# Kernel tuning notes

Measured on AMD Instinct MI355X. Metric: run time of the kernel, lower is better.

## Reference

```python
import jax, jax.numpy as jnp
import numpy as np

D_MODEL = 1024
NUM_HEADS = 16
D_K = D_MODEL // NUM_HEADS
THETA = 10000.0


def _rope(x, pos):
    # x: [B, H, T, d_k], pos: [T]
    inv_freq = 1.0 / (THETA ** (jnp.arange(0, D_K, 2, dtype=jnp.float32) / D_K))  # [d_k/2]
    ang = pos.astype(jnp.float32)[:, None] * inv_freq[None, :]                    # [T, d_k/2]
    cos = jnp.repeat(jnp.cos(ang), 2, axis=-1)                                    # [T, d_k]
    sin = jnp.repeat(jnp.sin(ang), 2, axis=-1)
    x = x.astype(jnp.float32)
    x0 = x[..., ::2]
    x1 = x[..., 1::2]
    rot = jnp.stack((-x1, x0), axis=-1).reshape(x.shape)  # rotate_half, interleaved
    return x * cos + rot * sin


def setup_inputs() -> dict:
    key = jax.random.key(0)
    k1, k2, k3 = jax.random.split(key, 3)
    B, T = 2, 2048
    sigma_qkv = float(np.sqrt(2.0 / (D_MODEL + 3 * D_MODEL)))
    sigma_out = float(np.sqrt(2.0 / (D_MODEL + D_MODEL)))
    return {
        "x": jax.random.normal(k1, (B, T, D_MODEL), dtype=jnp.float32),
        "w_qkv": jax.random.normal(k2, (3 * D_MODEL, D_MODEL), dtype=jnp.float32) * sigma_qkv,
        "w_out": jax.random.normal(k3, (D_MODEL, D_MODEL), dtype=jnp.float32) * sigma_out,
    }


def reference(x, w_qkv, w_out):
    B, T, _ = x.shape
    qkv = jnp.einsum("btd,ed->bte", x, w_qkv)                 # [B, T, 3*D]
    q, k, v = jnp.split(qkv, 3, axis=-1)

    def split_head(t):
        return t.reshape(B, T, NUM_HEADS, D_K).transpose(0, 2, 1, 3)  # [B, H, T, d_k]

    q, k, v = split_head(q), split_head(k), split_head(v)
    pos = jnp.arange(T)
    q = _rope(q, pos)
    k = _rope(k, pos)

    scores = jnp.einsum("bhqd,bhkd->bhqk", q, k) / jnp.sqrt(jnp.float32(D_K))
    causal = jnp.tril(jnp.ones((T, T), dtype=bool))            # True = keep
    scores = jnp.where(causal[None, None], scores, -jnp.inf)
    attn = jax.nn.softmax(scores, axis=-1)
    out = jnp.einsum("bhqk,bhkd->bhqd", attn, v)               # [B, H, T, d_k]
    out = out.transpose(0, 2, 1, 3).reshape(B, T, D_MODEL)
    return jnp.einsum("btd,ed->bte", out, w_out)
```

## Files before the change

### kernel.cpp

```cpp
#include <hip/hip_runtime.h>
#include <cstdint>
#include <cstddef>

#define BB 2
#define TT 2048
#define DMODEL 1024
#define NHEADS 16
#define DK 64

typedef short short8 __attribute__((ext_vector_type(8)));
typedef unsigned short ushort8 __attribute__((ext_vector_type(8)));
typedef float floatx4 __attribute__((ext_vector_type(4)));
typedef _Float16 half4 __attribute__((ext_vector_type(4)));
typedef float float2v __attribute__((ext_vector_type(2)));

#define MFMA_PV(A, B, C) __builtin_amdgcn_mfma_f32_16x16x16f16(A, B, C, 0, 0, 0)

__device__ __forceinline__ unsigned short f2bf(float f) {
    uint32_t u = __builtin_bit_cast(uint32_t, f);
    uint32_t r = (u + 0x7FFFu + ((u >> 16) & 1u)) >> 16;
    return (unsigned short)r;
}
__device__ __forceinline__ float bf2f(unsigned short s) {
    uint32_t u = ((uint32_t)s) << 16;
    return __builtin_bit_cast(float, u);
}

#define GLDS16(g, l) __builtin_amdgcn_global_load_lds( \
    (const __attribute__((address_space(1))) void*)(g), \
    (__attribute__((address_space(3))) void*)(l), 16, 0, 0)

__global__ void castk3(const float* __restrict__ x, unsigned short* __restrict__ xb,
                       const float* __restrict__ wq, unsigned short* __restrict__ wqb,
                       const float* __restrict__ wo, unsigned short* __restrict__ wob) {
    int bid = blockIdx.x;
    const float* in;
    unsigned short* out;
    int base;
    if (bid < 4096)       { in = x;  out = xb;  base = bid * 1024; }
    else if (bid < 7168)  { in = wq; out = wqb; base = (bid - 4096) * 1024; }
    else                  { in = wo; out = wob; base = (bid - 7168) * 1024; }
    int i = base + threadIdx.x * 4;
    float4 v = *(const float4*)(in + i);
    ushort4 o;
    o.x = f2bf(v.x); o.y = f2bf(v.y); o.z = f2bf(v.z); o.w = f2bf(v.w);
    *(ushort4*)(out + i) = o;
}

template <typename OUT>
__global__ __launch_bounds__(256)
void gemm_bt(const unsigned short* __restrict__ A, const unsigned short* __restrict__ B,
             OUT* __restrict__ C, int M, int N, int K) {
    __shared__ unsigned short As[128 * 32];
    __shared__ unsigned short Bs[128 * 32];

    const int tid  = threadIdx.x;
    const int lane = tid & 63;
    const int w    = tid >> 6;
    const int wm   = w & 1;
    const int wn   = w >> 1;
    const int quad = lane >> 4;
    const int l16  = lane & 15;

    const int m0 = blockIdx.y * 128;
    const int n0 = blockIdx.x * 128;

    floatx4 acc[4][4];
#pragma unroll
    for (int a = 0; a < 4; a++)
#pragma unroll
        for (int b = 0; b < 4; b++)
            acc[a][b] = (floatx4){0.f, 0.f, 0.f, 0.f};

    const int c0 = w * 128 + lane;
    const int c1 = c0 + 64;
    const int r0 = c0 >> 2, cc0 = (c0 & 3) ^ ((r0 >> 1) & 3);
    const int r1 = c1 >> 2, cc1 = (c1 & 3) ^ ((r1 >> 1) & 3);

    const unsigned short* gA0 = A + (size_t)(m0 + r0) * K + cc0 * 8;
    const unsigned short* gA1 = A + (size_t)(m0 + r1) * K + cc1 * 8;
    const unsigned short* gB0 = B + (size_t)(n0 + r0) * K + cc0 * 8;
    const unsigned short* gB1 = B + (size_t)(n0 + r1) * K + cc1 * 8;

    unsigned short* lA0 = &As[(2 * w + 0) * 512];
    unsigned short* lA1 = &As[(2 * w + 1) * 512];
    unsigned short* lB0 = &Bs[(2 * w + 0) * 512];
    unsigned short* lB1 = &Bs[(2 * w + 1) * 512];

    const int rsw = (l16 >> 1) & 3;

    for (int k0 = 0; k0 < K; k0 += 32) {
        __syncthreads();
        GLDS16(gA0 + k0, lA0);
        GLDS16(gA1 + k0, lA1);
        GLDS16(gB0 + k0, lB0);
        GLDS16(gB1 + k0, lB1);
        __syncthreads();

        short8 af[4], bf[4];
#pragma unroll
        for (int t = 0; t < 4; t++) {
            af[t] = *(const short8*)&As[(wm * 64 + t * 16 + l16) * 32 + (quad ^ rsw) * 8];
            bf[t] = *(const short8*)&Bs[(wn * 64 + t * 16 + l16) * 32 + (quad ^ rsw) * 8];
        }
#pragma unroll
        for (int tm = 0; tm < 4; tm++)
#pragma unroll
            for (int tn = 0; tn < 4; tn++)
                acc[tm][tn] = __builtin_amdgcn_mfma_f32_16x16x32_bf16(
                    af[tm], bf[tn], acc[tm][tn], 0, 0, 0);
    }

#pragma unroll
    for (int tm = 0; tm < 4; tm++) {
#pragma unroll
        for (int tn = 0; tn < 4; tn++) {
#pragma unroll
            for (int r = 0; r < 4; r++) {
                int m = m0 + wm * 64 + tm * 16 + quad * 4 + r;
                int n = n0 + wn * 64 + tn * 16 + l16;
                if constexpr (sizeof(OUT) == 4)
                    C[(size_t)m * N + n] = acc[tm][tn][r];
                else
                    C[(size_t)m * N + n] = f2bf(acc[tm][tn][r]);
            }
        }
    }
}

__global__ __launch_bounds__(512)
void gemm256(const unsigned short* __restrict__ A, const unsigned short* __restrict__ B,
             unsigned short* __restrict__ C, int M, int N, int K) {
    __shared__ unsigned short As[2][2][8192];
    __shared__ unsigned short Bs[2][2][8192];

    const int tid  = threadIdx.x;
    const int lane = tid & 63;
    const int w    = tid >> 6;
    const int wm   = w >> 2;
    const int wn   = w & 3;
    const int quad = lane >> 4;
    const int l16  = lane & 15;

    const int gx  = gridDim.x;
    const int bid = blockIdx.y * gx + blockIdx.x;
    const int cpx = (gx * gridDim.y) >> 3;
    const int wg  = (bid & 7) * cpx + (bid >> 3);
    const int m0  = (wg / gx) * 256;
    const int n0  = (wg % gx) * 256;

    floatx4 acc[8][4];
#pragma unroll
    for (int a = 0; a < 8; a++)
#pragma unroll
        for (int b = 0; b < 4; b++)
            acc[a][b] = (floatx4){0.f, 0.f, 0.f, 0.f};

    const int r1   = tid >> 3;
    const int koff = ((tid & 7) ^ (r1 & 7)) * 8;
    const unsigned short* Ag = A + (size_t)(m0 + r1) * K + koff;
    const unsigned short* Bg = B + (size_t)(n0 + r1) * K + koff;
    const int NT2 = K >> 6;

#define STAGE_A(dd, hh, kt) { \
    GLDS16(Ag + (size_t)((hh) * 128) * K + (kt) * 64,      &As[dd][hh][tid * 8]); \
    GLDS16(Ag + (size_t)((hh) * 128 + 64) * K + (kt) * 64, &As[dd][hh][4096 + tid * 8]); }
#define STAGE_B(dd, hh, kt) { \
    GLDS16(Bg + (size_t)((hh) * 128) * K + (kt) * 64,      &Bs[dd][hh][tid * 8]); \
    GLDS16(Bg + (size_t)((hh) * 128 + 64) * K + (kt) * 64, &Bs[dd][hh][4096 + tid * 8]); }

#define BARRIER() __builtin_amdgcn_s_barrier()

    STAGE_B(0, 0, 0); STAGE_B(0, 1, 0);
    STAGE_A(0, 0, 0); STAGE_A(0, 1, 0);
    STAGE_B(1, 0, 1); STAGE_B(1, 1, 1);
    asm volatile("s_waitcnt vmcnt(4)" ::: "memory");
    BARRIER();

    const int c0    = (quad ^ (l16 & 7)) * 8;
    const int bhalf = wn >> 1;
    const int brow0 = (wn & 1) * 64 + l16;

    short8 a[8], b[8];

    for (int it = 0; it < NT2; ++it) {
        const int d = it & 1;

#pragma unroll
        for (int nfl = 0; nfl < 2; nfl++)
#pragma unroll
            for (int ks = 0; ks < 2; ks++)
                b[2 * nfl + ks] = *(const short8*)&Bs[d][bhalf][(brow0 + nfl * 16) * 64 + (c0 ^ (ks * 32))];
#pragma unroll
        for (int mfl = 0; mfl < 4; mfl++)
#pragma unroll
            for (int ks = 0; ks < 2; ks++)
                a[2 * mfl + ks] = *(const short8*)&As[d][wm][(l16 + mfl * 16) * 64 + (c0 ^ (ks * 32))];
        if (it + 1 < NT2) STAGE_A(d ^ 1, 0, it + 1);
        BARRIER();
        __builtin_amdgcn_s_setprio(1);
#pragma unroll
        for (int mfl = 0; mfl < 4; mfl++)
#pragma unroll
            for (int nf = 0; nf < 2; nf++) {
                acc[mfl][nf] = __builtin_amdgcn_mfma_f32_16x16x32_bf16(a[2 * mfl], b[2 * nf], acc[mfl][nf], 0, 0, 0);
                acc[mfl][nf] = __builtin_amdgcn_mfma_f32_16x16x32_bf16(a[2 * mfl + 1], b[2 * nf + 1], acc[mfl][nf], 0, 0, 0);
            }
        __builtin_amdgcn_s_setprio(0);
        BARRIER();

#pragma unroll
        for (int nfl = 0; nfl < 2; nfl++)
#pragma unroll
            for (int ks = 0; ks < 2; ks++)
                b[4 + 2 * nfl + ks] = *(const short8*)&Bs[d][bhalf][(brow0 + 32 + nfl * 16) * 64 + (c0 ^ (ks * 32))];
        if (it + 1 < NT2) STAGE_A(d ^ 1, 1, it + 1);
        BARRIER();
        __builtin_amdgcn_s_setprio(1);
#pragma unroll
        for (int mfl = 0; mfl < 4; mfl++)
#pragma unroll
            for (int nf = 2; nf < 4; nf++) {
                acc[mfl][nf] = __builtin_amdgcn_mfma_f32_16x16x32_bf16(a[2 * mfl], b[2 * nf], acc[mfl][nf], 0, 0, 0);
                acc[mfl][nf] = __builtin_amdgcn_mfma_f32_16x16x32_bf16(a[2 * mfl + 1], b[2 * nf + 1], acc[mfl][nf], 0, 0, 0);
            }
        __builtin_amdgcn_s_setprio(0);
        BARRIER();

#pragma unroll
        for (int mfl = 0; mfl < 4; mfl++)
#pragma unroll
            for (int ks = 0; ks < 2; ks++)
                a[2 * mfl + ks] = *(const short8*)&As[d][wm][(64 + l16 + mfl * 16) * 64 + (c0 ^ (ks * 32))];
        if (it + 2 < NT2) STAGE_B(d, 0, it + 2);
        BARRIER();
        __builtin_amdgcn_s_setprio(1);
#pragma unroll
        for (int mfl = 0; mfl < 4; mfl++)
#pragma unroll
            for (int nf = 0; nf < 2; nf++) {
                acc[4 + mfl][nf] = __builtin_amdgcn_mfma_f32_16x16x32_bf16(a[2 * mfl], b[2 * nf], acc[4 + mfl][nf], 0, 0, 0);
                acc[4 + mfl][nf] = __builtin_amdgcn_mfma_f32_16x16x32_bf16(a[2 * mfl + 1], b[2 * nf + 1], acc[4 + mfl][nf], 0, 0, 0);
            }
        __builtin_amdgcn_s_setprio(0);
        BARRIER();

        if (it + 2 < NT2) STAGE_B(d, 1, it + 2);
        if (it < NT2 - 2) {
            asm volatile("s_waitcnt vmcnt(4)" ::: "memory");
        } else if (it == NT2 - 2) {
            asm volatile("s_waitcnt vmcnt(0)" ::: "memory");
        }
        BARRIER();
        __builtin_amdgcn_s_setprio(1);
#pragma unroll
        for (int mfl = 0; mfl < 4; mfl++)
#pragma unroll
            for (int nf = 2; nf < 4; nf++) {
                acc[4 + mfl][nf] = __builtin_amdgcn_mfma_f32_16x16x32_bf16(a[2 * mfl], b[2 * nf], acc[4 + mfl][nf], 0, 0, 0);
                acc[4 + mfl][nf] = __builtin_amdgcn_mfma_f32_16x16x32_bf16(a[2 * mfl + 1], b[2 * nf + 1], acc[4 + mfl][nf], 0, 0, 0);
            }
        __builtin_amdgcn_s_setprio(0);
        BARRIER();
    }
#undef STAGE_A
#undef STAGE_B
#undef BARRIER

#pragma unroll
    for (int mf = 0; mf < 8; mf++) {
#pragma unroll
        for (int nf = 0; nf < 4; nf++) {
#pragma unroll
            for (int r = 0; r < 4; r++) {
                int m = m0 + wm * 128 + mf * 16 + quad * 4 + r;
                int n = n0 + wn * 64 + nf * 16 + l16;
                C[(size_t)m * N + n] = f2bf(acc[mf][nf][r]);
            }
        }
    }
}

__global__ __launch_bounds__(256)
void ropevt(const unsigned short* __restrict__ qkv,
            unsigned short* __restrict__ qb, unsigned short* __restrict__ kb,
            unsigned short* __restrict__ vtb) {
    __shared__ unsigned short tile[64][72];
    const int tid = threadIdx.x;
    const int bh  = blockIdx.y;
    const int b = bh >> 4, h = bh & 15;
    const int t0 = blockIdx.x * 64;

    const float QS = 0.18033688f;
#pragma unroll
    for (int rep = 0; rep < 8; rep++) {
        int idx  = rep * 256 + tid;
        int p    = idx & 31;
        int trow = idx >> 5;
        int t    = t0 + trow;

        size_t src = (size_t)(b * TT + t) * 3072 + h * 64 + 2 * p;
        ushort2 qu = *(const ushort2*)(qkv + src);
        ushort2 ku = *(const ushort2*)(qkv + src + 1024);
        float qx = bf2f(qu.x), qy = bf2f(qu.y);
        float kx = bf2f(ku.x), ky = bf2f(ku.y);

        float invf = __powf(10000.f, -((float)(2 * p)) / 64.f);
        float ang  = (float)t * invf;
        float sn, cs;
        __sincosf(ang, &sn, &cs);

        size_t dst = ((size_t)bh * TT + t) * 64 + 2 * p;
        ushort2 qo, ko;
        qo.x = f2bf((qx * cs - qy * sn) * QS); qo.y = f2bf((qy * cs + qx * sn) * QS);
        ko.x = f2bf(kx * cs - ky * sn); ko.y = f2bf(ky * cs + kx * sn);
        *(ushort2*)(qb + dst) = qo;
        *(ushort2*)(kb + dst) = ko;
    }

    const int row = tid >> 2;
    const unsigned short* src = qkv + ((size_t)(b * TT) + t0 + row) * 3072 + 2048 + h * 64;
    {
        int cb = (tid & 3) * 16;
        ushort8 v0 = *(const ushort8*)(src + cb);
        ushort8 v1 = *(const ushort8*)(src + cb + 8);
#pragma unroll
        for (int i = 0; i < 8; i++) tile[row][cb + i] = v0[i];
#pragma unroll
        for (int i = 0; i < 8; i++) tile[row][cb + 8 + i] = v1[i];
    }
    __syncthreads();

    const int d  = tid >> 2;
    const int tc = tid & 3;
    const int hs = (d & 1) * 4;
    ushort8 o0, o1;
#pragma unroll
    for (int i = 0; i < 8; i++) {
        _Float16 hv = (_Float16)bf2f(tile[tc * 16 + (i ^ hs)][d]);
        o0[i] = __builtin_bit_cast(unsigned short, hv);
    }
#pragma unroll
    for (int i = 0; i < 8; i++) {
        _Float16 hv = (_Float16)bf2f(tile[tc * 16 + 8 + (i ^ hs)][d]);
        o1[i] = __builtin_bit_cast(unsigned short, hv);
    }
    unsigned short* dst = vtb + ((size_t)bh * 64 + d) * TT + t0 + tc * 16;
    *(ushort8*)(dst) = o0;
    *(ushort8*)(dst + 8) = o1;
}

__global__ __launch_bounds__(256, 3)
void attn_mfma(const unsigned short* __restrict__ qb,
               const unsigned short* __restrict__ kb,
               const unsigned short* __restrict__ vtb,
               unsigned short* __restrict__ out) {
    __shared__ unsigned short Ks[3][64 * 64];
    __shared__ unsigned short Vs[3][64 * 64];

    const int tid  = threadIdx.x;
    const int lane = tid & 63;
    const int w    = tid >> 6;
    const int quad = lane >> 4;
    const int l16  = lane & 15;

    const int bh    = blockIdx.x;
    const int qtile = gridDim.y - 1 - blockIdx.y;
    const int q0    = qtile * 64;

    const unsigned short* Qp = qb + ((size_t)bh * TT + q0 + w * 16) * 64;
    const unsigned short* Kp = kb + (size_t)bh * TT * 64;
    const unsigned short* Vp = vtb + (size_t)bh * 64 * TT;

    short8 aq[2];
#pragma unroll
    for (int ks = 0; ks < 2; ks++)
        aq[ks] = *(const short8*)(Qp + (size_t)l16 * 64 + ks * 32 + quad * 8);

    floatx4 Oacc[4];
#pragma unroll
    for (int dt = 0; dt < 4; dt++) Oacc[dt] = (floatx4){0.f, 0.f, 0.f, 0.f};
    floatx4 lacc = (floatx4){0.f, 0.f, 0.f, 0.f};

    const int ntiles = qtile + 1;

    const int cs0 = tid, cs1 = 256 + tid;
    const int rK0 = cs0 >> 3, sK0 = cs0 & 7;
    const int rK1 = cs1 >> 3, sK1 = cs1 & 7;
    const unsigned short* gk0 = Kp + rK0 * 64 + (sK0 ^ (rK0 & 7)) * 8;
    const unsigned short* gk1 = Kp + rK1 * 64 + (sK1 ^ (rK1 & 7)) * 8;
    const unsigned short* gv0 = Vp + (size_t)rK0 * TT + (sK0 ^ ((rK0 >> 1) & 7)) * 8;
    const unsigned short* gv1 = Vp + (size_t)rK1 * TT + (sK1 ^ ((rK1 >> 1) & 7)) * 8;
    const int ld0 = cs0 * 8, ld1 = cs1 * 8;

#define STAGE(IT, P)                                      \
    {                                                     \
        GLDS16(gk0 + (size_t)(IT) * 4096, &Ks[P][ld0]);   \
        GLDS16(gv0 + (IT) * 64,           &Vs[P][ld0]);   \
        GLDS16(gk1 + (size_t)(IT) * 4096, &Ks[P][ld1]);   \
        GLDS16(gv1 + (IT) * 64,           &Vs[P][ld1]);   \
    }

    STAGE(0, 0);
    if (ntiles > 1) {
        STAGE(1, 1);
        asm volatile("s_waitcnt vmcnt(4)" ::: "memory");
    } else {
        asm volatile("s_waitcnt vmcnt(0)" ::: "memory");
    }
    __builtin_amdgcn_s_barrier();

    const int ksw  = l16 & 7;
    const int vsw  = (l16 >> 1) & 7;
    const int vsub = ((quad & 1) ^ (l16 & 1)) * 4;
    const int kofs0 = (l16 * 64 + ((quad) ^ ksw) * 8) * 2;
    const int kofs1 = (l16 * 64 + ((4 + quad) ^ ksw) * 8) * 2;
    const int qh    = quad >> 1;
    const int vofs0 = (l16 * 64 + ((0 + qh) ^ vsw) * 8 + vsub) * 2;
    const int vofs1 = (l16 * 64 + ((2 + qh) ^ vsw) * 8 + vsub) * 2;
    const int vofs2 = (l16 * 64 + ((4 + qh) ^ vsw) * 8 + vsub) * 2;
    const int vofs3 = (l16 * 64 + ((6 + qh) ^ vsw) * 8 + vsub) * 2;

    const half4 vones = (half4){(_Float16)1.f, (_Float16)1.f, (_Float16)1.f, (_Float16)1.f};

    int p = 0, p2 = 2;

    for (int it = 0; it < ntiles; ++it) {
        if (it + 2 < ntiles) STAGE(it + 2, p2);

        const char* Kb = (const char*)Ks + p * 8192;
        const char* Vb = (const char*)Vs + p * 8192;

        floatx4 sacc[4];
#pragma unroll
        for (int nt = 0; nt < 4; nt++) sacc[nt] = (floatx4){0.f, 0.f, 0.f, 0.f};

#pragma unroll
        for (int ks = 0; ks < 2; ks++)
#pragma unroll
            for (int nt = 0; nt < 4; nt++) {
                short8 kf = *(const short8*)(Kb + (ks ? kofs1 : kofs0) + nt * 2048);
                sacc[nt] = __builtin_amdgcn_mfma_f32_16x16x32_bf16(kf, aq[ks], sacc[nt], 0, 0, 0);
            }

        if (it == qtile) {
            const int qg = w * 16 + l16;
#pragma unroll
            for (int nt = 0; nt < 4; nt++)
#pragma unroll
                for (int r = 0; r < 4; r++)
                    if (nt * 16 + quad * 4 + r > qg) sacc[nt][r] = -1e30f;
        }

#pragma unroll
        for (int nt = 0; nt < 4; nt++)
#pragma unroll
            for (int r = 0; r < 4; r++)
                sacc[nt][r] = __builtin_amdgcn_exp2f(sacc[nt][r]);

        half4 bp[4];
#pragma unroll
        for (int nt = 0; nt < 4; nt++) {
            float lo = __builtin_bit_cast(float, __builtin_amdgcn_cvt_pkrtz(sacc[nt][0], sacc[nt][1]));
            float hi = __builtin_bit_cast(float, __builtin_amdgcn_cvt_pkrtz(sacc[nt][2], sacc[nt][3]));
            float2v f2;
            f2[0] = lo;
            f2[1] = hi;
            bp[nt] = __builtin_bit_cast(half4, f2);
        }

        {
            floatx4 lsum;
#pragma unroll
            for (int r = 0; r < 4; r++)
                lsum[r] = (sacc[0][r] + sacc[1][r]) + (sacc[2][r] + sacc[3][r]);
            float llo = __builtin_bit_cast(float, __builtin_amdgcn_cvt_pkrtz(lsum[0], lsum[1]));
            float lhi = __builtin_bit_cast(float, __builtin_amdgcn_cvt_pkrtz(lsum[2], lsum[3]));
            float2v lf2;
            lf2[0] = llo;
            lf2[1] = lhi;
            half4 pl = __builtin_bit_cast(half4, lf2);
            lacc = MFMA_PV(vones, pl, lacc);
        }

#pragma unroll
        for (int dt = 0; dt < 4; dt++)
#pragma unroll
            for (int nt = 0; nt < 4; nt++) {
                const int vo = (nt == 0) ? vofs0 : (nt == 1) ? vofs1 : (nt == 2) ? vofs2 : vofs3;
                half4 vf = *(const half4*)(Vb + vo + dt * 2048);
                Oacc[dt] = MFMA_PV(vf, bp[nt], Oacc[dt]);
            }

        if (it + 1 < ntiles) {
            if (it + 2 < ntiles) {
                asm volatile("s_waitcnt vmcnt(4)" ::: "memory");
            } else {
                asm volatile("s_waitcnt vmcnt(0)" ::: "memory");
            }
            __builtin_amdgcn_s_barrier();
        }
        p  = (p == 2) ? 0 : p + 1;
        p2 = (p2 == 2) ? 0 : p2 + 1;
    }
#undef STAGE

    const int b = bh >> 4, h = bh & 15;
    const float inv = 1.f / lacc[0];
    const size_t base = ((size_t)(b * TT + q0 + w * 16 + l16)) * DMODEL + h * 64 + quad * 4;
#pragma unroll
    for (int dt = 0; dt < 4; dt++) {
        ushort4 pk;
        pk.x = f2bf(Oacc[dt][0] * inv);
        pk.y = f2bf(Oacc[dt][1] * inv);
        pk.z = f2bf(Oacc[dt][2] * inv);
        pk.w = f2bf(Oacc[dt][3] * inv);
        *(ushort4*)(out + base + dt * 16) = pk;
    }
}

extern "C" void kernel_launch(void* const* d_in, const int* in_sizes, int n_in,
                              void* d_out, int out_size, void* d_ws, size_t ws_size,
                              hipStream_t stream) {
    const float* x     = (const float*)d_in[0];
    const float* w_qkv = (const float*)d_in[1];
    const float* w_out = (const float*)d_in[2];
    float* out = (float*)d_out;

    char* ws = (char*)d_ws;

    unsigned short* xb   = (unsigned short*)(ws);
    unsigned short* wqb  = (unsigned short*)(ws + 8388608);
    unsigned short* wob  = (unsigned short*)(ws + 14680064);
    unsigned short* qkvb = (unsigned short*)(ws + 16777216);
    unsigned short* qb   = (unsigned short*)(ws + 41943040);
    unsigned short* kb   = (unsigned short*)(ws + 50331648);
    unsigned short* vtb  = (unsigned short*)(ws + 58720256);
    unsigned short* attb = (unsigned short*)(ws + 67108864);

    castk3<<<8192, 256, 0, stream>>>(x, xb, w_qkv, wqb, w_out, wob);

    gemm256<<<dim3(3072 / 256, 4096 / 256), 512, 0, stream>>>(
        xb, wqb, qkvb, 4096, 3072, 1024);

    ropevt<<<dim3(TT / 64, BB * NHEADS), 256, 0, stream>>>(qkvb, qb, kb, vtb);

    attn_mfma<<<dim3(BB * NHEADS, TT / 64), 256, 0, stream>>>(qb, kb, vtb, attb);

    gemm_bt<float><<<dim3(1024 / 128, 4096 / 128), 256, 0, stream>>>(
        attb, wob, out, 4096, 1024, 1024);
}
```

Before: 181.1 us.

## Process 128 queries per attention block to reuse K/V tiles across two subtiles

Each attention workgroup now handles a 128-query block, with each wave owning two 16-row query subtiles. Every K/V fragment loaded from LDS now feeds two MFMAs, which halves global K/V staging traffic and LDS reads per query. Causal masking is applied over the last two key tiles. The cost is more accumulator registers per wave (which may lower occupancy under launch_bounds 256,3), half as many blocks, and a few fully masked tile computations on the diagonal.

```diff
diff --git a/kernel.cpp b/kernel.cpp
--- a/kernel.cpp
+++ b/kernel.cpp
@@ -364,25 +364,31 @@
     const int quad = lane >> 4;
     const int l16  = lane & 15;
 
-    const int bh    = blockIdx.x;
-    const int qtile = gridDim.y - 1 - blockIdx.y;
-    const int q0    = qtile * 64;
-
-    const unsigned short* Qp = qb + ((size_t)bh * TT + q0 + w * 16) * 64;
+    const int bh   = blockIdx.x;
+    const int qblk = gridDim.y - 1 - blockIdx.y;
+    const int q0   = qblk * 128;
+
+    const unsigned short* Qp = qb + ((size_t)bh * TT + q0 + w * 32) * 64;
     const unsigned short* Kp = kb + (size_t)bh * TT * 64;
     const unsigned short* Vp = vtb + (size_t)bh * 64 * TT;
 
-    short8 aq[2];
-#pragma unroll
-    for (int ks = 0; ks < 2; ks++)
-        aq[ks] = *(const short8*)(Qp + (size_t)l16 * 64 + ks * 32 + quad * 8);
-
-    floatx4 Oacc[4];
-#pragma unroll
-    for (int dt = 0; dt < 4; dt++) Oacc[dt] = (floatx4){0.f, 0.f, 0.f, 0.f};
-    floatx4 lacc = (floatx4){0.f, 0.f, 0.f, 0.f};
-
-    const int ntiles = qtile + 1;
+    short8 aq[2][2];
+#pragma unroll
+    for (int s = 0; s < 2; s++)
+#pragma unroll
+        for (int ks = 0; ks < 2; ks++)
+            aq[s][ks] = *(const short8*)(Qp + (size_t)(s * 16 + l16) * 64 + ks * 32 + quad * 8);
+
+    floatx4 Oacc[2][4];
+#pragma unroll
+    for (int s = 0; s < 2; s++)
+#pragma unroll
+        for (int dt = 0; dt < 4; dt++) Oacc[s][dt] = (floatx4){0.f, 0.f, 0.f, 0.f};
+    floatx4 lacc[2];
+    lacc[0] = (floatx4){0.f, 0.f, 0.f, 0.f};
+    lacc[1] = (floatx4){0.f, 0.f, 0.f, 0.f};
+
+    const int ntiles = 2 * qblk + 2;
 
     const int cs0 = tid, cs1 = 256 + tid;
     const int rK0 = cs0 >> 3, sK0 = cs0 & 7;
@@ -402,12 +408,8 @@
     }
 
     STAGE(0, 0);
-    if (ntiles > 1) {
-        STAGE(1, 1);
-        asm volatile("s_waitcnt vmcnt(4)" ::: "memory");
-    } else {
-        asm volatile("s_waitcnt vmcnt(0)" ::: "memory");
-    }
+    STAGE(1, 1);
+    asm volatile("s_waitcnt vmcnt(4)" ::: "memory");
     __builtin_amdgcn_s_barrier();
 
     const int ksw  = l16 & 7;
@@ -431,56 +433,69 @@
         const char* Kb = (const char*)Ks + p * 8192;
         const char* Vb = (const char*)Vs + p * 8192;
 
-        floatx4 sacc[4];
-#pragma unroll
-        for (int nt = 0; nt < 4; nt++) sacc[nt] = (floatx4){0.f, 0.f, 0.f, 0.f};
+        floatx4 sacc[2][4];
+#pragma unroll
+        for (int s = 0; s < 2; s++)
+#pragma unroll
+            for (int nt = 0; nt < 4; nt++) sacc[s][nt] = (floatx4){0.f, 0.f, 0.f, 0.f};
 
 #pragma unroll
         for (int ks = 0; ks < 2; ks++)
 #pragma unroll
             for (int nt = 0; nt < 4; nt++) {
                 short8 kf = *(const short8*)(Kb + (ks ? kofs1 : kofs0) + nt * 2048);
-                sacc[nt] = __builtin_amdgcn_mfma_f32_16x16x32_bf16(kf, aq[ks], sacc[nt], 0, 0, 0);
-            }
-
-        if (it == qtile) {
-            const int qg = w * 16 + l16;
+#pragma unroll
+                for (int s = 0; s < 2; s++)
+                    sacc[s][nt] = __builtin_amdgcn_mfma_f32_16x16x32_bf16(kf, aq[s][ks], sacc[s][nt], 0, 0, 0);
+            }
+
+        if (it >= ntiles - 2) {
+            const int kbase = it * 64;
+#pragma unroll
+            for (int s = 0; s < 2; s++) {
+                const int qg = q0 + w * 32 + s * 16 + l16 - kbase;
+#pragma unroll
+                for (int nt = 0; nt < 4; nt++)
+#pragma unroll
+                    for (int r = 0; r < 4; r++)
+                        if (nt * 16 + quad * 4 + r > qg) sacc[s][nt][r] = -1e30f;
+            }
+        }
+
+#pragma unroll
+        for (int s = 0; s < 2; s++)
 #pragma unroll
             for (int nt = 0; nt < 4; nt++)
 #pragma unroll
                 for (int r = 0; r < 4; r++)
-                    if (nt * 16 + quad * 4 + r > qg) sacc[nt][r] = -1e30f;
-        }
-
-#pragma unroll
-        for (int nt = 0; nt < 4; nt++)
+                    sacc[s][nt][r] = __builtin_amdgcn_exp2f(sacc[s][nt][r]);
+
+        half4 bp[2][4];
+#pragma unroll
+        for (int s = 0; s < 2; s++)
+#pragma unroll
+            for (int nt = 0; nt < 4; nt++) {
+                float lo = __builtin_bit_cast(float, __builtin_amdgcn_cvt_pkrtz(sacc[s][nt][0], sacc[s][nt][1]));
+                float hi = __builtin_bit_cast(float, __builtin_amdgcn_cvt_pkrtz(sacc[s][nt][2], sacc[s][nt][3]));
+                float2v f2;
+                f2[0] = lo;
+                f2[1] = hi;
+                bp[s][nt] = __builtin_bit_cast(half4, f2);
+            }
+
+#pragma unroll
+        for (int s = 0; s < 2; s++) {
+            floatx4 lsum;
 #pragma unroll
             for (int r = 0; r < 4; r++)
-                sacc[nt][r] = __builtin_amdgcn_exp2f(sacc[nt][r]);
-
-        half4 bp[4];
-#pragma unroll
-        for (int nt = 0; nt < 4; nt++) {
-            float lo = __builtin_bit_cast(float, __builtin_amdgcn_cvt_pkrtz(sacc[nt][0], sacc[nt][1]));
-            float hi = __builtin_bit_cast(float, __builtin_amdgcn_cvt_pkrtz(sacc[nt][2], sacc[nt][3]));
-            float2v f2;
-            f2[0] = lo;
-            f2[1] = hi;
-            bp[nt] = __builtin_bit_cast(half4, f2);
-        }
-
-        {
-            floatx4 lsum;
-#pragma unroll
-            for (int r = 0; r < 4; r++)
-                lsum[r] = (sacc[0][r] + sacc[1][r]) + (sacc[2][r] + sacc[3][r]);
+                lsum[r] = (sacc[s][0][r] + sacc[s][1][r]) + (sacc[s][2][r] + sacc[s][3][r]);
             float llo = __builtin_bit_cast(float, __builtin_amdgcn_cvt_pkrtz(lsum[0], lsum[1]));
             float lhi = __builtin_bit_cast(float, __builtin_amdgcn_cvt_pkrtz(lsum[2], lsum[3]));
             float2v lf2;
             lf2[0] = llo;
             lf2[1] = lhi;
             half4 pl = __builtin_bit_cast(half4, lf2);
-            lacc = MFMA_PV(vones, pl, lacc);
+            lacc[s] = MFMA_PV(vones, pl, lacc[s]);
         }
 
 #pragma unroll
@@ -489,7 +504,9 @@
             for (int nt = 0; nt < 4; nt++) {
                 const int vo = (nt == 0) ? vofs0 : (nt == 1) ? vofs1 : (nt == 2) ? vofs2 : vofs3;
                 half4 vf = *(const half4*)(Vb + vo + dt * 2048);
-                Oacc[dt] = MFMA_PV(vf, bp[nt], Oacc[dt]);
+#pragma unroll
+                for (int s = 0; s < 2; s++)
+                    Oacc[s][dt] = MFMA_PV(vf, bp[s][nt], Oacc[s][dt]);
             }
 
         if (it + 1 < ntiles) {
@@ -506,16 +523,19 @@
 #undef STAGE
 
     const int b = bh >> 4, h = bh & 15;
-    const float inv = 1.f / lacc[0];
-    const size_t base = ((size_t)(b * TT + q0 + w * 16 + l16)) * DMODEL + h * 64 + quad * 4;
-#pragma unroll
-    for (int dt = 0; dt < 4; dt++) {
-        ushort4 pk;
-        pk.x = f2bf(Oacc[dt][0] * inv);
-        pk.y = f2bf(Oacc[dt][1] * inv);
-        pk.z = f2bf(Oacc[dt][2] * inv);
-        pk.w = f2bf(Oacc[dt][3] * inv);
-        *(ushort4*)(out + base + dt * 16) = pk;
+#pragma unroll
+    for (int s = 0; s < 2; s++) {
+        const float inv = 1.f / lacc[s][0];
+        const size_t base = ((size_t)(b * TT + q0 + w * 32 + s * 16 + l16)) * DMODEL + h * 64 + quad * 4;
+#pragma unroll
+        for (int dt = 0; dt < 4; dt++) {
+            ushort4 pk;
+            pk.x = f2bf(Oacc[s][dt][0] * inv);
+            pk.y = f2bf(Oacc[s][dt][1] * inv);
+            pk.z = f2bf(Oacc[s][dt][2] * inv);
+            pk.w = f2bf(Oacc[s][dt][3] * inv);
+            *(ushort4*)(out + base + dt * 16) = pk;
+        }
     }
 }
 
@@ -545,7 +565,7 @@
 
     ropevt<<<dim3(TT / 64, BB * NHEADS), 256, 0, stream>>>(qkvb, qb, kb, vtb);
 
-    attn_mfma<<<dim3(BB * NHEADS, TT / 64), 256, 0, stream>>>(qb, kb, vtb, attb);
+    attn_mfma<<<dim3(BB * NHEADS, TT / 128), 256, 0, stream>>>(qb, kb, vtb, attb);
 
     gemm_bt<float><<<dim3(1024 / 128, 4096 / 128), 256, 0, stream>>>(
         attb, wob, out, 4096, 1024, 1024);
```

Result: slower. 190.5 us (+5.2%).

## Enlarge attention query tile to 128 rows with 512-thread blocks

Applied to the files above, without the earlier changes.

The attention kernel now processes 128 query rows per block using 8 waves instead of 64 rows with 4 waves, so each staged K/V tile in shared memory is reused by twice as many waves. Each thread stages a single 16-byte chunk per K and V tile, and the wait counts are adjusted to match. The causal mask now applies to the last two KV tiles with a global-offset comparison. This halves K/V global traffic per query but creates fewer, larger blocks. It also wastes some compute on fully masked tiles for the lower-half waves and makes load imbalance coarser.

```diff
diff --git a/kernel.cpp b/kernel.cpp
--- a/kernel.cpp
+++ b/kernel.cpp
@@ -350,7 +350,7 @@
     *(ushort8*)(dst + 8) = o1;
 }
 
-__global__ __launch_bounds__(256, 3)
+__global__ __launch_bounds__(512, 4)
 void attn_mfma(const unsigned short* __restrict__ qb,
                const unsigned short* __restrict__ kb,
                const unsigned short* __restrict__ vtb,
@@ -364,9 +364,9 @@
     const int quad = lane >> 4;
     const int l16  = lane & 15;
 
-    const int bh    = blockIdx.x;
-    const int qtile = gridDim.y - 1 - blockIdx.y;
-    const int q0    = qtile * 64;
+    const int bh   = blockIdx.x;
+    const int qblk = gridDim.y - 1 - blockIdx.y;
+    const int q0   = qblk * 128;
 
     const unsigned short* Qp = qb + ((size_t)bh * TT + q0 + w * 16) * 64;
     const unsigned short* Kp = kb + (size_t)bh * TT * 64;
@@ -382,32 +382,22 @@
     for (int dt = 0; dt < 4; dt++) Oacc[dt] = (floatx4){0.f, 0.f, 0.f, 0.f};
     floatx4 lacc = (floatx4){0.f, 0.f, 0.f, 0.f};
 
-    const int ntiles = qtile + 1;
-
-    const int cs0 = tid, cs1 = 256 + tid;
-    const int rK0 = cs0 >> 3, sK0 = cs0 & 7;
-    const int rK1 = cs1 >> 3, sK1 = cs1 & 7;
-    const unsigned short* gk0 = Kp + rK0 * 64 + (sK0 ^ (rK0 & 7)) * 8;
-    const unsigned short* gk1 = Kp + rK1 * 64 + (sK1 ^ (rK1 & 7)) * 8;
-    const unsigned short* gv0 = Vp + (size_t)rK0 * TT + (sK0 ^ ((rK0 >> 1) & 7)) * 8;
-    const unsigned short* gv1 = Vp + (size_t)rK1 * TT + (sK1 ^ ((rK1 >> 1) & 7)) * 8;
-    const int ld0 = cs0 * 8, ld1 = cs1 * 8;
-
-#define STAGE(IT, P)                                      \
-    {                                                     \
-        GLDS16(gk0 + (size_t)(IT) * 4096, &Ks[P][ld0]);   \
-        GLDS16(gv0 + (IT) * 64,           &Vs[P][ld0]);   \
-        GLDS16(gk1 + (size_t)(IT) * 4096, &Ks[P][ld1]);   \
-        GLDS16(gv1 + (IT) * 64,           &Vs[P][ld1]);   \
+    const int ntiles = 2 * qblk + 2;
+
+    const int rK = tid >> 3, sK = tid & 7;
+    const unsigned short* gk = Kp + rK * 64 + (sK ^ (rK & 7)) * 8;
+    const unsigned short* gv = Vp + (size_t)rK * TT + (sK ^ ((rK >> 1) & 7)) * 8;
+    const int ld = tid * 8;
+
+#define STAGE(IT, P)                                     \
+    {                                                    \
+        GLDS16(gk + (size_t)(IT) * 4096, &Ks[P][ld]);    \
+        GLDS16(gv + (IT) * 64,           &Vs[P][ld]);    \
     }
 
     STAGE(0, 0);
-    if (ntiles > 1) {
-        STAGE(1, 1);
-        asm volatile("s_waitcnt vmcnt(4)" ::: "memory");
-    } else {
-        asm volatile("s_waitcnt vmcnt(0)" ::: "memory");
-    }
+    STAGE(1, 1);
+    asm volatile("s_waitcnt vmcnt(2)" ::: "memory");
     __builtin_amdgcn_s_barrier();
 
     const int ksw  = l16 & 7;
@@ -443,8 +433,8 @@
                 sacc[nt] = __builtin_amdgcn_mfma_f32_16x16x32_bf16(kf, aq[ks], sacc[nt], 0, 0, 0);
             }
 
-        if (it == qtile) {
-            const int qg = w * 16 + l16;
+        if (it >= ntiles - 2) {
+            const int qg = q0 + w * 16 + l16 - it * 64;
 #pragma unroll
             for (int nt = 0; nt < 4; nt++)
 #pragma unroll
@@ -494,7 +484,7 @@
 
         if (it + 1 < ntiles) {
             if (it + 2 < ntiles) {
-                asm volatile("s_waitcnt vmcnt(4)" ::: "memory");
+                asm volatile("s_waitcnt vmcnt(2)" ::: "memory");
             } else {
                 asm volatile("s_waitcnt vmcnt(0)" ::: "memory");
             }
@@ -545,7 +535,7 @@
 
     ropevt<<<dim3(TT / 64, BB * NHEADS), 256, 0, stream>>>(qkvb, qb, kb, vtb);
 
-    attn_mfma<<<dim3(BB * NHEADS, TT / 64), 256, 0, stream>>>(qb, kb, vtb, attb);
+    attn_mfma<<<dim3(BB * NHEADS, TT / 128), 512, 0, stream>>>(qb, kb, vtb, attb);
 
     gemm_bt<float><<<dim3(1024 / 128, 4096 / 128), 256, 0, stream>>>(
         attb, wob, out, 4096, 1024, 1024);
```

Measured after the change: 189.3 us. 1.05x slower.

## Replace pipelined 256x256 QKV GEMM with simpler 256x128 single-buffered tile kernel

Applied to the files above, without the earlier changes.

The QKV projection GEMM drops the 256x256 tile with double-buffered LDS, split-phase barriers and MFMA priority hints. It becomes a 256x128 tile kernel with K-step 32, a single LDS buffer and a plain load/sync/compute loop. The grid doubles to 384 blocks, which fills more CUs and uses less LDS per block. In exchange it loses the overlap of global loads with MFMA work and has lower arithmetic intensity per tile.

```diff
diff --git a/kernel.cpp b/kernel.cpp
--- a/kernel.cpp
+++ b/kernel.cpp
@@ -129,16 +129,16 @@
 }
 
 __global__ __launch_bounds__(512)
-void gemm256(const unsigned short* __restrict__ A, const unsigned short* __restrict__ B,
+void gemm_mn(const unsigned short* __restrict__ A, const unsigned short* __restrict__ B,
              unsigned short* __restrict__ C, int M, int N, int K) {
-    __shared__ unsigned short As[2][2][8192];
-    __shared__ unsigned short Bs[2][2][8192];
+    __shared__ unsigned short As[256 * 32];
+    __shared__ unsigned short Bs[128 * 32];
 
     const int tid  = threadIdx.x;
     const int lane = tid & 63;
     const int w    = tid >> 6;
-    const int wm   = w >> 2;
-    const int wn   = w & 3;
+    const int wm   = w & 3;
+    const int wn   = w >> 2;
     const int quad = lane >> 4;
     const int l16  = lane & 15;
 
@@ -147,135 +147,59 @@
     const int cpx = (gx * gridDim.y) >> 3;
     const int wg  = (bid & 7) * cpx + (bid >> 3);
     const int m0  = (wg / gx) * 256;
-    const int n0  = (wg % gx) * 256;
-
-    floatx4 acc[8][4];
-#pragma unroll
-    for (int a = 0; a < 8; a++)
+    const int n0  = (wg % gx) * 128;
+
+    floatx4 acc[4][4];
+#pragma unroll
+    for (int a = 0; a < 4; a++)
 #pragma unroll
         for (int b = 0; b < 4; b++)
             acc[a][b] = (floatx4){0.f, 0.f, 0.f, 0.f};
 
-    const int r1   = tid >> 3;
-    const int koff = ((tid & 7) ^ (r1 & 7)) * 8;
-    const unsigned short* Ag = A + (size_t)(m0 + r1) * K + koff;
-    const unsigned short* Bg = B + (size_t)(n0 + r1) * K + koff;
-    const int NT2 = K >> 6;
-
-#define STAGE_A(dd, hh, kt) { \
-    GLDS16(Ag + (size_t)((hh) * 128) * K + (kt) * 64,      &As[dd][hh][tid * 8]); \
-    GLDS16(Ag + (size_t)((hh) * 128 + 64) * K + (kt) * 64, &As[dd][hh][4096 + tid * 8]); }
-#define STAGE_B(dd, hh, kt) { \
-    GLDS16(Bg + (size_t)((hh) * 128) * K + (kt) * 64,      &Bs[dd][hh][tid * 8]); \
-    GLDS16(Bg + (size_t)((hh) * 128 + 64) * K + (kt) * 64, &Bs[dd][hh][4096 + tid * 8]); }
-
-#define BARRIER() __builtin_amdgcn_s_barrier()
-
-    STAGE_B(0, 0, 0); STAGE_B(0, 1, 0);
-    STAGE_A(0, 0, 0); STAGE_A(0, 1, 0);
-    STAGE_B(1, 0, 1); STAGE_B(1, 1, 1);
-    asm volatile("s_waitcnt vmcnt(4)" ::: "memory");
-    BARRIER();
-
-    const int c0    = (quad ^ (l16 & 7)) * 8;
-    const int bhalf = wn >> 1;
-    const int brow0 = (wn & 1) * 64 + l16;
-
-    short8 a[8], b[8];
-
-    for (int it = 0; it < NT2; ++it) {
-        const int d = it & 1;
-
-#pragma unroll
-        for (int nfl = 0; nfl < 2; nfl++)
-#pragma unroll
-            for (int ks = 0; ks < 2; ks++)
-                b[2 * nfl + ks] = *(const short8*)&Bs[d][bhalf][(brow0 + nfl * 16) * 64 + (c0 ^ (ks * 32))];
-#pragma unroll
-        for (int mfl = 0; mfl < 4; mfl++)
-#pragma unroll
-            for (int ks = 0; ks < 2; ks++)
-                a[2 * mfl + ks] = *(const short8*)&As[d][wm][(l16 + mfl * 16) * 64 + (c0 ^ (ks * 32))];
-        if (it + 1 < NT2) STAGE_A(d ^ 1, 0, it + 1);
-        BARRIER();
-        __builtin_amdgcn_s_setprio(1);
-#pragma unroll
-        for (int mfl = 0; mfl < 4; mfl++)
-#pragma unroll
-            for (int nf = 0; nf < 2; nf++) {
-                acc[mfl][nf] = __builtin_amdgcn_mfma_f32_16x16x32_bf16(a[2 * mfl], b[2 * nf], acc[mfl][nf], 0, 0, 0);
-                acc[mfl][nf] = __builtin_amdgcn_mfma_f32_16x16x32_bf16(a[2 * mfl + 1], b[2 * nf + 1], acc[mfl][nf], 0, 0, 0);
-            }
-        __builtin_amdgcn_s_setprio(0);
-        BARRIER();
-
-#pragma unroll
-        for (int nfl = 0; nfl < 2; nfl++)
-#pragma unroll
-            for (int ks = 0; ks < 2; ks++)
-                b[4 + 2 * nfl + ks] = *(const short8*)&Bs[d][bhalf][(brow0 + 32 + nfl * 16) * 64 + (c0 ^ (ks * 32))];
-        if (it + 1 < NT2) STAGE_A(d ^ 1, 1, it + 1);
-        BARRIER();
-        __builtin_amdgcn_s_setprio(1);
-#pragma unroll
-        for (int mfl = 0; mfl < 4; mfl++)
-#pragma unroll
-            for (int nf = 2; nf < 4; nf++) {
-                acc[mfl][nf] = __builtin_amdgcn_mfma_f32_16x16x32_bf16(a[2 * mfl], b[2 * nf], acc[mfl][nf], 0, 0, 0);
-                acc[mfl][nf] = __builtin_amdgcn_mfma_f32_16x16x32_bf16(a[2 * mfl + 1], b[2 * nf + 1], acc[mfl][nf], 0, 0, 0);
-            }
-        __builtin_amdgcn_s_setprio(0);
-        BARRIER();
-
-#pragma unroll
-        for (int mfl = 0; mfl < 4; mfl++)
-#pragma unroll
-            for (int ks = 0; ks < 2; ks++)
-                a[2 * mfl + ks] = *(const short8*)&As[d][wm][(64 + l16 + mfl * 16) * 64 + (c0 ^ (ks * 32))];
-        if (it + 2 < NT2) STAGE_B(d, 0, it + 2);
-        BARRIER();
-        __builtin_amdgcn_s_setprio(1);
-#pragma unroll
-        for (int mfl = 0; mfl < 4; mfl++)
-#pragma unroll
-            for (int nf = 0; nf < 2; nf++) {
-                acc[4 + mfl][nf] = __builtin_amdgcn_mfma_f32_16x16x32_bf16(a[2 * mfl], b[2 * nf], acc[4 + mfl][nf], 0, 0, 0);
-                acc[4 + mfl][nf] = __builtin_amdgcn_mfma_f32_16x16x32_bf16(a[2 * mfl + 1], b[2 * nf + 1], acc[4 + mfl][nf], 0, 0, 0);
-            }
-        __builtin_amdgcn_s_setprio(0);
-        BARRIER();
-
-        if (it + 2 < NT2) STAGE_B(d, 1, it + 2);
-        if (it < NT2 - 2) {
-            asm volatile("s_waitcnt vmcnt(4)" ::: "memory");
-        } else if (it == NT2 - 2) {
-            asm volatile("s_waitcnt vmcnt(0)" ::: "memory");
-        }
-        BARRIER();
-        __builtin_amdgcn_s_setprio(1);
-#pragma unroll
-        for (int mfl = 0; mfl < 4; mfl++)
-#pragma unroll
-            for (int nf = 2; nf < 4; nf++) {
-                acc[4 + mfl][nf] = __builtin_amdgcn_mfma_f32_16x16x32_bf16(a[2 * mfl], b[2 * nf], acc[4 + mfl][nf], 0, 0, 0);
-                acc[4 + mfl][nf] = __builtin_amdgcn_mfma_f32_16x16x32_bf16(a[2 * mfl + 1], b[2 * nf + 1], acc[4 + mfl][nf], 0, 0, 0);
-            }
-        __builtin_amdgcn_s_setprio(0);
-        BARRIER();
-    }
-#undef STAGE_A
-#undef STAGE_B
-#undef BARRIER
-
-#pragma unroll
-    for (int mf = 0; mf < 8; mf++) {
-#pragma unroll
-        for (int nf = 0; nf < 4; nf++) {
+    const int ca0 = tid,       ra0 = ca0 >> 2, cca0 = (ca0 & 3) ^ ((ra0 >> 1) & 3);
+    const int ca1 = tid + 512, ra1 = ca1 >> 2, cca1 = (ca1 & 3) ^ ((ra1 >> 1) & 3);
+    const int rb  = tid >> 2,  ccb  = (tid & 3) ^ ((rb >> 1) & 3);
+
+    const unsigned short* gA0 = A + (size_t)(m0 + ra0) * K + cca0 * 8;
+    const unsigned short* gA1 = A + (size_t)(m0 + ra1) * K + cca1 * 8;
+    const unsigned short* gB0 = B + (size_t)(n0 + rb) * K + ccb * 8;
+
+    unsigned short* lA0 = &As[ca0 * 8];
+    unsigned short* lA1 = &As[ca1 * 8];
+    unsigned short* lB0 = &Bs[tid * 8];
+
+    const int rsw = (l16 >> 1) & 3;
+
+    for (int k0 = 0; k0 < K; k0 += 32) {
+        __syncthreads();
+        GLDS16(gA0 + k0, lA0);
+        GLDS16(gA1 + k0, lA1);
+        GLDS16(gB0 + k0, lB0);
+        __syncthreads();
+
+        short8 af[4], bf[4];
+#pragma unroll
+        for (int t = 0; t < 4; t++) {
+            af[t] = *(const short8*)&As[(wm * 64 + t * 16 + l16) * 32 + (quad ^ rsw) * 8];
+            bf[t] = *(const short8*)&Bs[(wn * 64 + t * 16 + l16) * 32 + (quad ^ rsw) * 8];
+        }
+#pragma unroll
+        for (int tm = 0; tm < 4; tm++)
+#pragma unroll
+            for (int tn = 0; tn < 4; tn++)
+                acc[tm][tn] = __builtin_amdgcn_mfma_f32_16x16x32_bf16(
+                    af[tm], bf[tn], acc[tm][tn], 0, 0, 0);
+    }
+
+#pragma unroll
+    for (int tm = 0; tm < 4; tm++) {
+#pragma unroll
+        for (int tn = 0; tn < 4; tn++) {
 #pragma unroll
             for (int r = 0; r < 4; r++) {
-                int m = m0 + wm * 128 + mf * 16 + quad * 4 + r;
-                int n = n0 + wn * 64 + nf * 16 + l16;
-                C[(size_t)m * N + n] = f2bf(acc[mf][nf][r]);
+                int m = m0 + wm * 64 + tm * 16 + quad * 4 + r;
+                int n = n0 + wn * 64 + tn * 16 + l16;
+                C[(size_t)m * N + n] = f2bf(acc[tm][tn][r]);
             }
         }
     }
@@ -540,7 +464,7 @@
 
     castk3<<<8192, 256, 0, stream>>>(x, xb, w_qkv, wqb, w_out, wob);
 
-    gemm256<<<dim3(3072 / 256, 4096 / 256), 512, 0, stream>>>(
+    gemm_mn<<<dim3(3072 / 128, 4096 / 256), 512, 0, stream>>>(
         xb, wqb, qkvb, 4096, 3072, 1024);
 
     ropevt<<<dim3(TT / 64, BB * NHEADS), 256, 0, stream>>>(qkvb, qb, kb, vtb);
```

Result: no change. 183.9 us (+1.6%).
